# Optimization experiments

Measured on AMD Instinct MI355X. Metric: run time of the kernel, lower is better.

Reference implementation:

```python
import jax, jax.numpy as jnp
import numpy as np

B = 2_097_152          # batch of theta samples
POLY_DEG = 127         # QSP polynomial degree -> 128 phases
PI = np.float32(np.pi)


def setup_inputs() -> dict:
    key = jax.random.key(0)
    k1, k2 = jax.random.split(key)
    th = jax.random.uniform(k1, (B, 1), dtype=jnp.float32) * PI
    phis = jax.random.uniform(k2, (POLY_DEG + 1, 1), dtype=jnp.float32) * PI
    return {"th": th, "phis": phis}


def reference(th, phis):
    # th: [B,1] float32, phis: [P+1,1] float32 (learned QSP phases)
    theta = th[:, 0]                      # [B]
    c = jnp.cos(theta)
    s = jnp.sin(theta)
    # expm(i*theta*X) = cos(theta) I + i sin(theta) X  (closed form, no expm)
    wx = jnp.stack(
        [jnp.stack([c + 0j, 1j * s], axis=-1),
         jnp.stack([1j * s, c + 0j], axis=-1)],
        axis=-2,
    ).astype(jnp.complex64)               # [B,2,2]

    phi = phis[:, 0]                      # [P+1]
    e = jnp.exp(1j * phi).astype(jnp.complex64)
    # expm(i*phi*Z) = diag(e^{i phi}, e^{-i phi})
    rz = (jnp.zeros((phi.shape[0], 2, 2), jnp.complex64)
          .at[:, 0, 0].set(e)
          .at[:, 1, 1].set(jnp.conj(e)))  # [P+1,2,2]

    u0 = jnp.broadcast_to(rz[0], (theta.shape[0], 2, 2))  # [B,2,2]

    def step(u, rzk):
        u = jnp.einsum('bij,bjk->bik', u, wx)   # u @ W(x)
        u = jnp.einsum('bij,jk->bik', u, rzk)   # ... @ Rz(phi_k)
        return u, None

    u, _ = jax.lax.scan(step, u0, rz[1:])       # 127 sequential steps
    # convention == 0: (Re[u_00], Im[u_00])
    return (jnp.real(u[:, 0, 0]), jnp.imag(u[:, 0, 0]))
```

## Files before the change

### kernel.cpp

```cpp
#include <hip/hip_runtime.h>


typedef float v2f __attribute__((ext_vector_type(2)));

#define NPHI 128

__global__ __launch_bounds__(1024, 8) void qsp_fused(
    const float* __restrict__ th,
    const float* __restrict__ phis,
    float* __restrict__ out,
    int Bq)
{
    __shared__ float2 g2[NPHI];
    __shared__ float2 h[NPHI];

    const int tid = threadIdx.x;

    if (tid < 64) {
        const int L = tid;
        float sp, cp;
        __sincosf(phis[L], &sp, &cp);
        h[L] = make_float2(0.5f * cp, 0.5f * sp);
        __sincosf(phis[L + 64], &sp, &cp);
        h[L + 64] = make_float2(0.5f * cp, 0.5f * sp);

        v2f A0 = {0.f, 0.f}, B0 = {0.f, 0.f};
        v2f A1 = {0.f, 0.f}, B1 = {0.f, 0.f};
        const float2 h0 = h[0];
        if (L == 0) A0 = (v2f){2.f * h0.x, 2.f * h0.y};

        #pragma unroll 4
        for (int k = 1; k < NPHI; ++k) {
            const float2 hk = h[k];
            const v2f hx  = {hk.x, hk.x};
            const v2f hyn = {-hk.y, hk.y};
            const v2f hyp = {hk.y, -hk.y};
            const float pAr = __shfl_up(A1.x, 1, 64);
            const float pAi = __shfl_up(A1.y, 1, 64);
            const float pBr = __shfl_up(B1.x, 1, 64);
            const float pBi = __shfl_up(B1.y, 1, 64);
            v2f pA = {pAr, pAi}, pB = {pBr, pBi};
            if (L == 0) { pA = (v2f){0.f, 0.f}; pB = (v2f){0.f, 0.f}; }
            const v2f u0 = pA + pB, v0 = A0 - B0;
            const v2f sA0 = u0 + v0, sB0 = u0 - v0;
            const v2f u1 = A0 + B0, v1 = A1 - B1;
            const v2f sA1 = u1 + v1, sB1 = u1 - v1;
            v2f ts;
            ts = (v2f){sA0.y, sA0.x};
            A0 = __builtin_elementwise_fma(hyn, ts, hx * sA0);
            ts = (v2f){sB0.y, sB0.x};
            B0 = __builtin_elementwise_fma(hyp, ts, hx * sB0);
            ts = (v2f){sA1.y, sA1.x};
            A1 = __builtin_elementwise_fma(hyn, ts, hx * sA1);
            ts = (v2f){sB1.y, sB1.x};
            B1 = __builtin_elementwise_fma(hyp, ts, hx * sB1);
        }
        g2[2 * L]     = make_float2(A0.x, A0.y);
        g2[2 * L + 1] = make_float2(A1.x, A1.y);
    }

    const int idx = blockIdx.x * blockDim.x + tid;
    const int lidx = (idx < Bq) ? idx : 0;
    const float4 t4 = ((const float4*)th)[lidx];

    float zs0, zc0, zs1, zc1, zs2, zc2, zs3, zc3;
    __sincosf(2.f * t4.x, &zs0, &zc0);
    __sincosf(2.f * t4.y, &zs1, &zc1);
    __sincosf(2.f * t4.z, &zs2, &zc2);
    __sincosf(2.f * t4.w, &zs3, &zc3);
    const v2f zrA = {zc0, zc1}, ziA = {zs0, zs1}, nziA = {-zs0, -zs1};
    const v2f zrB = {zc2, zc3}, ziB = {zs2, zs3}, nziB = {-zs2, -zs3};

    float S0, C0, S1, C1, S2, C2, S3, C3;
    __sincosf(127.f * t4.x, &S0, &C0);
    __sincosf(127.f * t4.y, &S1, &C1);
    __sincosf(127.f * t4.z, &S2, &C2);
    __sincosf(127.f * t4.w, &S3, &C3);

    __syncthreads();

    const float2 gt = g2[NPHI - 1];
    v2f arA = {gt.x, gt.x}, aiA = {gt.y, gt.y};
    v2f arB = arA,          aiB = aiA;

    #pragma unroll 4
    for (int j = NPHI - 2; j >= 0; --j) {
        const float2 gj = g2[j];
        const v2f gr = {gj.x, gj.x};
        const v2f gi = {gj.y, gj.y};
        const v2f nrA = __builtin_elementwise_fma(
            arA, zrA, __builtin_elementwise_fma(aiA, nziA, gr));
        const v2f niA = __builtin_elementwise_fma(
            arA, ziA, __builtin_elementwise_fma(aiA, zrA, gi));
        const v2f nrB = __builtin_elementwise_fma(
            arB, zrB, __builtin_elementwise_fma(aiB, nziB, gr));
        const v2f niB = __builtin_elementwise_fma(
            arB, ziB, __builtin_elementwise_fma(aiB, zrB, gi));
        arA = nrA; aiA = niA;
        arB = nrB; aiB = niB;
    }

    const v2f CA = {C0, C1}, SA = {S0, S1};
    const v2f CB = {C2, C3}, SB = {S2, S3};
    const v2f orA = __builtin_elementwise_fma(arA, CA, aiA * SA);
    const v2f oiA = __builtin_elementwise_fma(aiA, CA, -(arA * SA));
    const v2f orB = __builtin_elementwise_fma(arB, CB, aiB * SB);
    const v2f oiB = __builtin_elementwise_fma(aiB, CB, -(arB * SB));

    if (idx < Bq) {
        ((float4*)out)[idx]      = make_float4(orA.x, orA.y, orB.x, orB.y);
        ((float4*)out)[idx + Bq] = make_float4(oiA.x, oiA.y, oiB.x, oiB.y);
    }
}

extern "C" void kernel_launch(void* const* d_in, const int* in_sizes, int n_in,
                              void* d_out, int out_size, void* d_ws, size_t ws_size,
                              hipStream_t stream)
{
    const float* th   = (const float*)d_in[0];
    const float* phis = (const float*)d_in[1];
    float* out = (float*)d_out;
    const int B = in_sizes[0];
    const int Bq = B >> 2;
    const int block = 1024;
    const int grid = (Bq + block - 1) / block;
    qsp_fused<<<grid, block, 0, stream>>>(th, phis, out, Bq);
}
```

Before: 89.91 us.

## Process eight thetas per thread, use DPP shift, and paired LDS coefficient loads

Each thread now evaluates the Horner recurrence for eight samples instead of four, so each LDS coefficient load is shared across more FMAs and the block shrinks to 512 threads. The coefficient table is read as float4 pairs to halve LDS load instructions. The wavefront shuffle in the phase-precompute step is replaced with a DPP row-shift builtin to avoid ds_bpermute traffic. This adds register pressure and changes the launch shape, and the DPP control 0x138 may not match the cross-lane semantics of the original shuffle (zero fill for lane 0, full 64-lane shift).

```diff
diff --git a/kernel.cpp b/kernel.cpp
--- a/kernel.cpp
+++ b/kernel.cpp
@@ -5,13 +5,19 @@
 
 #define NPHI 128
 
-__global__ __launch_bounds__(1024, 8) void qsp_fused(
+__device__ __forceinline__ float wave_shr1(float x) {
+    return __builtin_bit_cast(float,
+        __builtin_amdgcn_update_dpp(0, __builtin_bit_cast(int, x),
+                                    0x138, 0xf, 0xf, true));
+}
+
+__global__ __launch_bounds__(512, 4) void qsp_fused(
     const float* __restrict__ th,
     const float* __restrict__ phis,
     float* __restrict__ out,
-    int Bq)
+    int Bq8)
 {
-    __shared__ float2 g2[NPHI];
+    __shared__ alignas(16) float2 g2[NPHI];
     __shared__ float2 h[NPHI];
 
     const int tid = threadIdx.x;
@@ -35,12 +41,8 @@
             const v2f hx  = {hk.x, hk.x};
             const v2f hyn = {-hk.y, hk.y};
             const v2f hyp = {hk.y, -hk.y};
-            const float pAr = __shfl_up(A1.x, 1, 64);
-            const float pAi = __shfl_up(A1.y, 1, 64);
-            const float pBr = __shfl_up(B1.x, 1, 64);
-            const float pBi = __shfl_up(B1.y, 1, 64);
-            v2f pA = {pAr, pAi}, pB = {pBr, pBi};
-            if (L == 0) { pA = (v2f){0.f, 0.f}; pB = (v2f){0.f, 0.f}; }
+            const v2f pA = { wave_shr1(A1.x), wave_shr1(A1.y) };
+            const v2f pB = { wave_shr1(B1.x), wave_shr1(B1.y) };
             const v2f u0 = pA + pB, v0 = A0 - B0;
             const v2f sA0 = u0 + v0, sB0 = u0 - v0;
             const v2f u1 = A0 + B0, v1 = A1 - B1;
@@ -60,56 +62,73 @@
     }
 
     const int idx = blockIdx.x * blockDim.x + tid;
-    const int lidx = (idx < Bq) ? idx : 0;
-    const float4 t4 = ((const float4*)th)[lidx];
+    const int lidx = (idx < Bq8) ? idx : 0;
+    const float4 ta = ((const float4*)th)[2 * lidx];
+    const float4 tb = ((const float4*)th)[2 * lidx + 1];
+    const float th8[8] = {ta.x, ta.y, ta.z, ta.w, tb.x, tb.y, tb.z, tb.w};
 
-    float zs0, zc0, zs1, zc1, zs2, zc2, zs3, zc3;
-    __sincosf(2.f * t4.x, &zs0, &zc0);
-    __sincosf(2.f * t4.y, &zs1, &zc1);
-    __sincosf(2.f * t4.z, &zs2, &zc2);
-    __sincosf(2.f * t4.w, &zs3, &zc3);
-    const v2f zrA = {zc0, zc1}, ziA = {zs0, zs1}, nziA = {-zs0, -zs1};
-    const v2f zrB = {zc2, zc3}, ziB = {zs2, zs3}, nziB = {-zs2, -zs3};
-
-    float S0, C0, S1, C1, S2, C2, S3, C3;
-    __sincosf(127.f * t4.x, &S0, &C0);
-    __sincosf(127.f * t4.y, &S1, &C1);
-    __sincosf(127.f * t4.z, &S2, &C2);
-    __sincosf(127.f * t4.w, &S3, &C3);
+    v2f zr[4], zi[4], nzi[4], Cc[4], Ss[4];
+    #pragma unroll
+    for (int g = 0; g < 4; ++g) {
+        float s0, c0, s1, c1;
+        __sincosf(2.f * th8[2 * g],     &s0, &c0);
+        __sincosf(2.f * th8[2 * g + 1], &s1, &c1);
+        zr[g]  = (v2f){c0, c1};
+        zi[g]  = (v2f){s0, s1};
+        nzi[g] = (v2f){-s0, -s1};
+        __sincosf(127.f * th8[2 * g],     &s0, &c0);
+        __sincosf(127.f * th8[2 * g + 1], &s1, &c1);
+        Cc[g] = (v2f){c0, c1};
+        Ss[g] = (v2f){s0, s1};
+    }
 
     __syncthreads();
 
-    const float2 gt = g2[NPHI - 1];
-    v2f arA = {gt.x, gt.x}, aiA = {gt.y, gt.y};
-    v2f arB = arA,          aiB = aiA;
+    v2f ar[4] = {{0.f,0.f},{0.f,0.f},{0.f,0.f},{0.f,0.f}};
+    v2f ai[4] = {{0.f,0.f},{0.f,0.f},{0.f,0.f},{0.f,0.f}};
+    const float4* g4 = (const float4*)g2;
 
     #pragma unroll 4
-    for (int j = NPHI - 2; j >= 0; --j) {
-        const float2 gj = g2[j];
-        const v2f gr = {gj.x, gj.x};
-        const v2f gi = {gj.y, gj.y};
-        const v2f nrA = __builtin_elementwise_fma(
-            arA, zrA, __builtin_elementwise_fma(aiA, nziA, gr));
-        const v2f niA = __builtin_elementwise_fma(
-            arA, ziA, __builtin_elementwise_fma(aiA, zrA, gi));
-        const v2f nrB = __builtin_elementwise_fma(
-            arB, zrB, __builtin_elementwise_fma(aiB, nziB, gr));
-        const v2f niB = __builtin_elementwise_fma(
-            arB, ziB, __builtin_elementwise_fma(aiB, zrB, gi));
-        arA = nrA; aiA = niA;
-        arB = nrB; aiB = niB;
+    for (int jj = NPHI / 2 - 1; jj >= 0; --jj) {
+        const float4 gp = g4[jj];
+        {
+            const v2f gr = {gp.z, gp.z}, gi = {gp.w, gp.w};
+            #pragma unroll
+            for (int g = 0; g < 4; ++g) {
+                const v2f nr = __builtin_elementwise_fma(
+                    ar[g], zr[g], __builtin_elementwise_fma(ai[g], nzi[g], gr));
+                const v2f ni = __builtin_elementwise_fma(
+                    ar[g], zi[g], __builtin_elementwise_fma(ai[g], zr[g], gi));
+                ar[g] = nr; ai[g] = ni;
+            }
+        }
+        {
+            const v2f gr = {gp.x, gp.x}, gi = {gp.y, gp.y};
+            #pragma unroll
+            for (int g = 0; g < 4; ++g) {
+                const v2f nr = __builtin_elementwise_fma(
+                    ar[g], zr[g], __builtin_elementwise_fma(ai[g], nzi[g], gr));
+                const v2f ni = __builtin_elementwise_fma(
+                    ar[g], zi[g], __builtin_elementwise_fma(ai[g], zr[g], gi));
+                ar[g] = nr; ai[g] = ni;
+            }
+        }
     }
 
-    const v2f CA = {C0, C1}, SA = {S0, S1};
-    const v2f CB = {C2, C3}, SB = {S2, S3};
-    const v2f orA = __builtin_elementwise_fma(arA, CA, aiA * SA);
-    const v2f oiA = __builtin_elementwise_fma(aiA, CA, -(arA * SA));
-    const v2f orB = __builtin_elementwise_fma(arB, CB, aiB * SB);
-    const v2f oiB = __builtin_elementwise_fma(aiB, CB, -(arB * SB));
+    v2f orv[4], oiv[4];
+    #pragma unroll
+    for (int g = 0; g < 4; ++g) {
+        orv[g] = __builtin_elementwise_fma(ar[g], Cc[g], ai[g] * Ss[g]);
+        oiv[g] = __builtin_elementwise_fma(ai[g], Cc[g], -(ar[g] * Ss[g]));
+    }
 
-    if (idx < Bq) {
-        ((float4*)out)[idx]      = make_float4(orA.x, orA.y, orB.x, orB.y);
-        ((float4*)out)[idx + Bq] = make_float4(oiA.x, oiA.y, oiB.x, oiB.y);
+    if (idx < Bq8) {
+        float4* o4 = (float4*)out;
+        const int ib = 2 * Bq8;
+        o4[2 * idx]          = make_float4(orv[0].x, orv[0].y, orv[1].x, orv[1].y);
+        o4[2 * idx + 1]      = make_float4(orv[2].x, orv[2].y, orv[3].x, orv[3].y);
+        o4[ib + 2 * idx]     = make_float4(oiv[0].x, oiv[0].y, oiv[1].x, oiv[1].y);
+        o4[ib + 2 * idx + 1] = make_float4(oiv[2].x, oiv[2].y, oiv[3].x, oiv[3].y);
     }
 }
 
@@ -121,8 +140,8 @@
     const float* phis = (const float*)d_in[1];
     float* out = (float*)d_out;
     const int B = in_sizes[0];
-    const int Bq = B >> 2;
-    const int block = 1024;
-    const int grid = (Bq + block - 1) / block;
-    qsp_fused<<<grid, block, 0, stream>>>(th, phis, out, Bq);
+    const int Bq8 = B >> 3;
+    const int block = 512;
+    const int grid = (Bq8 + block - 1) / block;
+    qsp_fused<<<grid, block, 0, stream>>>(th, phis, out, Bq8);
 }
```

Measured after the change: 88.12 us. -2.0%, faster.
